# Optimization experiments

Hardware: AMD Instinct MI355X
Metric: run time of the kernel (lower is better)

Reference implementation:

```python
import jax, jax.numpy as jnp
import numpy as np

N = 8192
PERCEPTION = 0.2
SEP_DIST = 0.02
ACC_SCALE = 1.0
ACC_MAX = 1.0
EPS = 1e-08


def setup_inputs() -> dict:
    key = jax.random.key(0)
    k1, k2, k3 = jax.random.split(key, 3)
    position = jax.random.uniform(k1, (N, 2), dtype=jnp.float32)  # boids live in [0,1]^2 torus
    velocity = jax.random.normal(k2, (N, 2), dtype=jnp.float32) * 0.05
    noise = jax.random.uniform(k3, (N, 2), dtype=jnp.float32, minval=-1.0, maxval=1.0)
    return {
        "position": position,
        "velocity": velocity,
        "noise": noise,
        "separation_weight": jnp.float32(4.5),
        "alignment_weight": jnp.float32(0.65),
        "cohesion_weight": jnp.float32(0.75),
        "noise_scale": jnp.float32(0.05),
    }


def _normalize(v):
    # per-row normalize, matching module's _normalize
    norm = jnp.maximum(jnp.linalg.norm(v, axis=-1, keepdims=True), EPS)
    return v / norm


def reference(position, velocity, noise, separation_weight, alignment_weight, cohesion_weight, noise_scale):
    # Toroidal vector from boid i to boid j: diff[i, j, :]  (shape [N, N, 2])
    diff = position[None, :, :] - position[:, None, :]
    diff = jnp.where(diff > 0.5, diff - 1.0, diff)
    diff = jnp.where(diff < -0.5, diff + 1.0, diff)
    dist2 = jnp.sum(diff * diff, axis=-1)  # [N, N]

    not_self = ~jnp.eye(N, dtype=bool)

    # Separation: sum of -toroidal_vector over too-close neighbors, normalized
    sep_mask = not_self & (dist2 <= SEP_DIST ** 2)
    steer_sep = -jnp.sum(jnp.where(sep_mask[..., None], diff, 0.0), axis=1)
    steer_sep = _normalize(steer_sep)

    # Perception mask shared by alignment and cohesion
    perc_mask = not_self & (dist2 <= PERCEPTION ** 2)
    cnt = jnp.sum(perc_mask, axis=1, dtype=position.dtype)[:, None]  # [N, 1]

    # Alignment: mean neighbor velocity minus own velocity, normalized
    vel_avg = jnp.einsum("ij,jd->id", perc_mask.astype(position.dtype), velocity) / cnt
    steer_align = _normalize(vel_avg - velocity)

    # Cohesion: mean toroidal vector to neighbors, normalized
    pos_avg = jnp.sum(jnp.where(perc_mask[..., None], diff, 0.0), axis=1) / cnt
    steer_coh = _normalize(pos_avg)

    acc = (separation_weight * steer_sep
           + alignment_weight * steer_align
           + cohesion_weight * steer_coh)
    acc = acc * ACC_SCALE
    acc = acc + noise_scale * noise

    # clip by norm per boid
    norm = jnp.linalg.norm(acc, axis=-1, keepdims=True)
    acc = jnp.where(norm > ACC_MAX, acc * ACC_MAX / jnp.maximum(norm, EPS), acc)
    return acc
```

## Files before the change

### kernel.cpp

```cpp
#include <hip/hip_runtime.h>
#include <math.h>

#define N_BOIDS 8192
typedef float f32x2 __attribute__((ext_vector_type(2)));
typedef float f32x4 __attribute__((ext_vector_type(4)));

constexpr int   BLOCK           = 256;
constexpr int   WAVES_PER_BLOCK = BLOCK / 64;
constexpr int   I_PER_WAVE      = 2;
constexpr int   I_PER_BLOCK     = WAVES_PER_BLOCK * I_PER_WAVE;
constexpr int   TILE            = 2048;
constexpr int   NTILES          = N_BOIDS / TILE;
constexpr float SEP_R2  = 4.0000000000000008e-04f;
constexpr float PERC_R2 = 4.0000000000000001e-02f;
constexpr float EPSF    = 1e-08f;

__device__ __forceinline__ void finalize_boid(
    int i, const f32x2* __restrict__ vel, const f32x2* __restrict__ noise,
    float ws, float wa, float wc, float wn,
    float sx, float sy, float vx, float vy, float cx, float cy, float cntall,
    float* __restrict__ out)
{
    const float cnt = cntall - 1.0f;

    float ns  = fmaxf(sqrtf(sx * sx + sy * sy), EPSF);
    float ssx = sx / ns, ssy = sy / ns;

    const f32x2 vi = vel[i];
    float vax = (vx - vi.x) / cnt - vi.x;
    float vay = (vy - vi.y) / cnt - vi.y;
    float na  = fmaxf(sqrtf(vax * vax + vay * vay), EPSF);
    float sax = vax / na, say = vay / na;

    float pax = cx / cnt, pay = cy / cnt;
    float nc  = fmaxf(sqrtf(pax * pax + pay * pay), EPSF);
    float scx = pax / nc, scy = pay / nc;

    float ax = ws * ssx + wa * sax + wc * scx;
    float ay = ws * ssy + wa * say + wc * scy;
    const f32x2 nz = noise[i];
    ax += wn * nz.x;
    ay += wn * nz.y;

    const float nn = sqrtf(ax * ax + ay * ay);
    if (nn > 1.0f) {
        const float s = 1.0f / fmaxf(nn, EPSF);
        ax *= s;
        ay *= s;
    }
    out[2 * i]     = ax;
    out[2 * i + 1] = ay;
}

__global__ __launch_bounds__(BLOCK, 4) void boids_kernel(
    const f32x2* __restrict__ pos,
    const f32x2* __restrict__ vel,
    const f32x2* __restrict__ noise,
    const float* __restrict__ w_sep,
    const float* __restrict__ w_ali,
    const float* __restrict__ w_coh,
    const float* __restrict__ w_noise,
    float* __restrict__ out)
{
    __shared__ f32x4 tile[TILE];

    const int tid  = threadIdx.x;
    const int lane = tid & 63;
    const int wid  = tid >> 6;
    const int i0   = (blockIdx.x * WAVES_PER_BLOCK + wid) * I_PER_WAVE;

    const f32x2 P0 = pos[i0];
    const f32x2 P1 = pos[i0 + 1];
    const float vperc = PERC_R2;
    const float vsep  = SEP_R2;

    float n0 = 0.f, s0x = 0.f, s0y = 0.f, v0x = 0.f, v0y = 0.f, c0x = 0.f, c0y = 0.f;
    float n1 = 0.f, s1x = 0.f, s1y = 0.f, v1x = 0.f, v1y = 0.f, c1x = 0.f, c1y = 0.f;

    for (int t = 0; t < NTILES; ++t) {
        const f32x4* gp = reinterpret_cast<const f32x4*>(pos) + t * (TILE / 2);
        const f32x4* gv = reinterpret_cast<const f32x4*>(vel) + t * (TILE / 2);
#pragma unroll
        for (int c = 0; c < TILE / 2 / BLOCK; ++c) {
            const int idx  = tid + c * BLOCK;
            const f32x4 pp = gp[idx];
            const f32x4 vv = gv[idx];
            f32x4 t0; t0.x = pp.x; t0.y = pp.y; t0.z = vv.x; t0.w = vv.y;
            f32x4 t1; t1.x = pp.z; t1.y = pp.w; t1.z = vv.z; t1.w = vv.w;
            tile[2 * idx]     = t0;
            tile[2 * idx + 1] = t1;
        }
        __syncthreads();

#pragma unroll 8
        for (int k = 0; k < TILE / 64; ++k) {
            const f32x4 q = tile[lane + k * 64];
            float dx, dy, ta, tb, m;
            asm(
                "v_sub_f32   %[dx], %[qx], %[p0x]\n\t"
                "v_sub_f32   %[dy], %[qy], %[p0y]\n\t"
                "v_rndne_f32 %[ta], %[dx]\n\t"
                "v_rndne_f32 %[tb], %[dy]\n\t"
                "v_sub_f32   %[dx], %[dx], %[ta]\n\t"
                "v_sub_f32   %[dy], %[dy], %[tb]\n\t"
                "v_mul_f32   %[ta], %[dx], %[dx]\n\t"
                "v_mul_f32   %[tb], %[dy], %[dy]\n\t"
                "v_add_f32   %[ta], %[ta], %[tb]\n\t"
                "v_cmp_ge_f32 vcc, %[vperc], %[ta]\n\t"
                "v_cndmask_b32 %[m], 0, 1.0, vcc\n\t"
                "v_add_f32   %[n0], %[n0], %[m]\n\t"
                "v_fmac_f32  %[v0x], %[m], %[qz]\n\t"
                "v_fmac_f32  %[v0y], %[m], %[qw]\n\t"
                "v_fmac_f32  %[c0x], %[m], %[dx]\n\t"
                "v_fmac_f32  %[c0y], %[m], %[dy]\n\t"
                "v_cmp_ge_f32 vcc, %[vsep], %[ta]\n\t"
                "v_cndmask_b32 %[m], 0, 1.0, vcc\n\t"
                "v_fma_f32   %[s0x], -%[m], %[dx], %[s0x]\n\t"
                "v_fma_f32   %[s0y], -%[m], %[dy], %[s0y]\n\t"
                "v_sub_f32   %[dx], %[qx], %[p1x]\n\t"
                "v_sub_f32   %[dy], %[qy], %[p1y]\n\t"
                "v_rndne_f32 %[ta], %[dx]\n\t"
                "v_rndne_f32 %[tb], %[dy]\n\t"
                "v_sub_f32   %[dx], %[dx], %[ta]\n\t"
                "v_sub_f32   %[dy], %[dy], %[tb]\n\t"
                "v_mul_f32   %[ta], %[dx], %[dx]\n\t"
                "v_mul_f32   %[tb], %[dy], %[dy]\n\t"
                "v_add_f32   %[ta], %[ta], %[tb]\n\t"
                "v_cmp_ge_f32 vcc, %[vperc], %[ta]\n\t"
                "v_cndmask_b32 %[m], 0, 1.0, vcc\n\t"
                "v_add_f32   %[n1], %[n1], %[m]\n\t"
                "v_fmac_f32  %[v1x], %[m], %[qz]\n\t"
                "v_fmac_f32  %[v1y], %[m], %[qw]\n\t"
                "v_fmac_f32  %[c1x], %[m], %[dx]\n\t"
                "v_fmac_f32  %[c1y], %[m], %[dy]\n\t"
                "v_cmp_ge_f32 vcc, %[vsep], %[ta]\n\t"
                "v_cndmask_b32 %[m], 0, 1.0, vcc\n\t"
                "v_fma_f32   %[s1x], -%[m], %[dx], %[s1x]\n\t"
                "v_fma_f32   %[s1y], -%[m], %[dy], %[s1y]\n\t"
                : [dx] "=&v"(dx), [dy] "=&v"(dy), [ta] "=&v"(ta),
                  [tb] "=&v"(tb), [m] "=&v"(m),
                  [n0] "+v"(n0), [s0x] "+v"(s0x), [s0y] "+v"(s0y),
                  [v0x] "+v"(v0x), [v0y] "+v"(v0y), [c0x] "+v"(c0x), [c0y] "+v"(c0y),
                  [n1] "+v"(n1), [s1x] "+v"(s1x), [s1y] "+v"(s1y),
                  [v1x] "+v"(v1x), [v1y] "+v"(v1y), [c1x] "+v"(c1x), [c1y] "+v"(c1y)
                : [qx] "v"(q.x), [qy] "v"(q.y), [qz] "v"(q.z), [qw] "v"(q.w),
                  [p0x] "v"(P0.x), [p0y] "v"(P0.y),
                  [p1x] "v"(P1.x), [p1y] "v"(P1.y),
                  [vperc] "v"(vperc), [vsep] "v"(vsep)
                : "vcc");
        }
        __syncthreads();
    }

#pragma unroll
    for (int mlev = 1; mlev < 64; mlev <<= 1) {
        n0  += __shfl_xor(n0,  mlev);
        s0x += __shfl_xor(s0x, mlev);  s0y += __shfl_xor(s0y, mlev);
        v0x += __shfl_xor(v0x, mlev);  v0y += __shfl_xor(v0y, mlev);
        c0x += __shfl_xor(c0x, mlev);  c0y += __shfl_xor(c0y, mlev);
        n1  += __shfl_xor(n1,  mlev);
        s1x += __shfl_xor(s1x, mlev);  s1y += __shfl_xor(s1y, mlev);
        v1x += __shfl_xor(v1x, mlev);  v1y += __shfl_xor(v1y, mlev);
        c1x += __shfl_xor(c1x, mlev);  c1y += __shfl_xor(c1y, mlev);
    }

    float sx = s0x, sy = s0y, vx = v0x, vy = v0y, cx = c0x, cy = c0y, cc = n0;
    if (lane == 1) {
        sx = s1x; sy = s1y; vx = v1x; vy = v1y; cx = c1x; cy = c1y; cc = n1;
    }
    if (lane < I_PER_WAVE) {
        const float ws = w_sep[0], wa = w_ali[0], wc = w_coh[0], wn = w_noise[0];
        finalize_boid(i0 + lane, vel, noise, ws, wa, wc, wn,
                      sx, sy, vx, vy, cx, cy, cc, out);
    }
}

extern "C" void kernel_launch(void* const* d_in, const int* in_sizes, int n_in,
                              void* d_out, int out_size, void* d_ws, size_t ws_size,
                              hipStream_t stream) {
    const f32x2* pos     = (const f32x2*)d_in[0];
    const f32x2* vel     = (const f32x2*)d_in[1];
    const f32x2* noise   = (const f32x2*)d_in[2];
    const float* w_sep   = (const float*)d_in[3];
    const float* w_ali   = (const float*)d_in[4];
    const float* w_coh   = (const float*)d_in[5];
    const float* w_noise = (const float*)d_in[6];
    float* out = (float*)d_out;

    const int grid = N_BOIDS / I_PER_BLOCK;
    boids_kernel<<<grid, BLOCK, 0, stream>>>(pos, vel, noise, w_sep, w_ali,
                                             w_coh, w_noise, out);
}
```

Before: 34.26 us.

## Split neighbor loop across wave pairs and branch-skip sparse separation updates

```diff
diff --git a/kernel.cpp b/kernel.cpp
--- a/kernel.cpp
+++ b/kernel.cpp
@@ -5,12 +5,14 @@
 typedef float f32x2 __attribute__((ext_vector_type(2)));
 typedef float f32x4 __attribute__((ext_vector_type(4)));
 
-constexpr int   BLOCK           = 256;
-constexpr int   WAVES_PER_BLOCK = BLOCK / 64;
-constexpr int   I_PER_WAVE      = 2;
-constexpr int   I_PER_BLOCK     = WAVES_PER_BLOCK * I_PER_WAVE;
-constexpr int   TILE            = 2048;
-constexpr int   NTILES          = N_BOIDS / TILE;
+constexpr int   BLOCK       = 1024;
+constexpr int   JSPLIT      = 2;
+constexpr int   GROUPS      = (BLOCK / 64) / JSPLIT;
+constexpr int   I_PER_GROUP = 2;
+constexpr int   I_PER_BLOCK = GROUPS * I_PER_GROUP;
+constexpr int   TILE        = 4096;
+constexpr int   NTILES      = N_BOIDS / TILE;
+constexpr int   K_PER_WAVE  = TILE / 64 / JSPLIT;
 constexpr float SEP_R2  = 4.0000000000000008e-04f;
 constexpr float PERC_R2 = 4.0000000000000001e-02f;
 constexpr float EPSF    = 1e-08f;
@@ -52,7 +54,7 @@
     out[2 * i + 1] = ay;
 }
 
-__global__ __launch_bounds__(BLOCK, 4) void boids_kernel(
+__global__ __launch_bounds__(BLOCK, 8) void boids_kernel(
     const f32x2* __restrict__ pos,
     const f32x2* __restrict__ vel,
     const f32x2* __restrict__ noise,
@@ -63,19 +65,22 @@
     float* __restrict__ out)
 {
     __shared__ f32x4 tile[TILE];
+    __shared__ float comb[GROUPS][16];
 
     const int tid  = threadIdx.x;
     const int lane = tid & 63;
     const int wid  = tid >> 6;
-    const int i0   = (blockIdx.x * WAVES_PER_BLOCK + wid) * I_PER_WAVE;
+    const int g    = wid >> 1;
+    const int h    = wid & 1;
+    const int i0   = blockIdx.x * I_PER_BLOCK + g * I_PER_GROUP;
 
     const f32x2 P0 = pos[i0];
     const f32x2 P1 = pos[i0 + 1];
     const float vperc = PERC_R2;
     const float vsep  = SEP_R2;
 
-    float n0 = 0.f, s0x = 0.f, s0y = 0.f, v0x = 0.f, v0y = 0.f, c0x = 0.f, c0y = 0.f;
-    float n1 = 0.f, s1x = 0.f, s1y = 0.f, v1x = 0.f, v1y = 0.f, c1x = 0.f, c1y = 0.f;
+    float n0  = 0.f, s0x = 0.f, s0y = 0.f, v0x = 0.f, v0y = 0.f, c0x = 0.f, c0y = 0.f;
+    float n1  = 0.f, s1x = 0.f, s1y = 0.f, v1x = 0.f, v1y = 0.f, c1x = 0.f, c1y = 0.f;
 
     for (int t = 0; t < NTILES; ++t) {
         const f32x4* gp = reinterpret_cast<const f32x4*>(pos) + t * (TILE / 2);
@@ -92,62 +97,71 @@
         }
         __syncthreads();
 
+        const int kbase = h * K_PER_WAVE;
 #pragma unroll 8
-        for (int k = 0; k < TILE / 64; ++k) {
-            const f32x4 q = tile[lane + k * 64];
-            float dx, dy, ta, tb, m;
+        for (int k = 0; k < K_PER_WAVE; ++k) {
+            const f32x4 q = tile[lane + (kbase + k) * 64];
+            float dx0, dy0, dx1, dy1, ta, tb, tc, m;
+            unsigned long long ka, kb, kc;
             asm(
-                "v_sub_f32   %[dx], %[qx], %[p0x]\n\t"
-                "v_sub_f32   %[dy], %[qy], %[p0y]\n\t"
-                "v_rndne_f32 %[ta], %[dx]\n\t"
-                "v_rndne_f32 %[tb], %[dy]\n\t"
-                "v_sub_f32   %[dx], %[dx], %[ta]\n\t"
-                "v_sub_f32   %[dy], %[dy], %[tb]\n\t"
-                "v_mul_f32   %[ta], %[dx], %[dx]\n\t"
-                "v_mul_f32   %[tb], %[dy], %[dy]\n\t"
+                "v_sub_f32   %[dx0], %[qx], %[p0x]\n\t"
+                "v_sub_f32   %[dy0], %[qy], %[p0y]\n\t"
+                "v_sub_f32   %[dx1], %[qx], %[p1x]\n\t"
+                "v_sub_f32   %[dy1], %[qy], %[p1y]\n\t"
+                "v_rndne_f32 %[ta], %[dx0]\n\t"
+                "v_rndne_f32 %[tb], %[dy0]\n\t"
+                "v_sub_f32   %[dx0], %[dx0], %[ta]\n\t"
+                "v_sub_f32   %[dy0], %[dy0], %[tb]\n\t"
+                "v_rndne_f32 %[ta], %[dx1]\n\t"
+                "v_rndne_f32 %[tb], %[dy1]\n\t"
+                "v_sub_f32   %[dx1], %[dx1], %[ta]\n\t"
+                "v_sub_f32   %[dy1], %[dy1], %[tb]\n\t"
+                "v_mul_f32   %[ta], %[dx0], %[dx0]\n\t"
+                "v_mul_f32   %[tb], %[dy0], %[dy0]\n\t"
                 "v_add_f32   %[ta], %[ta], %[tb]\n\t"
+                "v_mul_f32   %[tb], %[dx1], %[dx1]\n\t"
+                "v_mul_f32   %[tc], %[dy1], %[dy1]\n\t"
+                "v_add_f32   %[tb], %[tb], %[tc]\n\t"
                 "v_cmp_ge_f32 vcc, %[vperc], %[ta]\n\t"
                 "v_cndmask_b32 %[m], 0, 1.0, vcc\n\t"
                 "v_add_f32   %[n0], %[n0], %[m]\n\t"
                 "v_fmac_f32  %[v0x], %[m], %[qz]\n\t"
                 "v_fmac_f32  %[v0y], %[m], %[qw]\n\t"
-                "v_fmac_f32  %[c0x], %[m], %[dx]\n\t"
-                "v_fmac_f32  %[c0y], %[m], %[dy]\n\t"
-                "v_cmp_ge_f32 vcc, %[vsep], %[ta]\n\t"
-                "v_cndmask_b32 %[m], 0, 1.0, vcc\n\t"
-                "v_fma_f32   %[s0x], -%[m], %[dx], %[s0x]\n\t"
-                "v_fma_f32   %[s0y], -%[m], %[dy], %[s0y]\n\t"
-                "v_sub_f32   %[dx], %[qx], %[p1x]\n\t"
-                "v_sub_f32   %[dy], %[qy], %[p1y]\n\t"
-                "v_rndne_f32 %[ta], %[dx]\n\t"
-                "v_rndne_f32 %[tb], %[dy]\n\t"
-                "v_sub_f32   %[dx], %[dx], %[ta]\n\t"
-                "v_sub_f32   %[dy], %[dy], %[tb]\n\t"
-                "v_mul_f32   %[ta], %[dx], %[dx]\n\t"
-                "v_mul_f32   %[tb], %[dy], %[dy]\n\t"
-                "v_add_f32   %[ta], %[ta], %[tb]\n\t"
-                "v_cmp_ge_f32 vcc, %[vperc], %[ta]\n\t"
+                "v_fmac_f32  %[c0x], %[m], %[dx0]\n\t"
+                "v_fmac_f32  %[c0y], %[m], %[dy0]\n\t"
+                "v_cmp_ge_f32 vcc, %[vperc], %[tb]\n\t"
                 "v_cndmask_b32 %[m], 0, 1.0, vcc\n\t"
                 "v_add_f32   %[n1], %[n1], %[m]\n\t"
                 "v_fmac_f32  %[v1x], %[m], %[qz]\n\t"
                 "v_fmac_f32  %[v1y], %[m], %[qw]\n\t"
-                "v_fmac_f32  %[c1x], %[m], %[dx]\n\t"
-                "v_fmac_f32  %[c1y], %[m], %[dy]\n\t"
-                "v_cmp_ge_f32 vcc, %[vsep], %[ta]\n\t"
-                "v_cndmask_b32 %[m], 0, 1.0, vcc\n\t"
-                "v_fma_f32   %[s1x], -%[m], %[dx], %[s1x]\n\t"
-                "v_fma_f32   %[s1y], -%[m], %[dy], %[s1y]\n\t"
-                : [dx] "=&v"(dx), [dy] "=&v"(dy), [ta] "=&v"(ta),
-                  [tb] "=&v"(tb), [m] "=&v"(m),
+                "v_fmac_f32  %[c1x], %[m], %[dx1]\n\t"
+                "v_fmac_f32  %[c1y], %[m], %[dy1]\n\t"
+                "v_cmp_ge_f32 %[ka], %[vsep], %[ta]\n\t"
+                "v_cmp_ge_f32 %[kb], %[vsep], %[tb]\n\t"
+                "s_or_b64    %[kc], %[ka], %[kb]\n\t"
+                "s_cbranch_scc0 Lsep%=\n\t"
+                "v_cndmask_b32 %[m], 0, 1.0, %[ka]\n\t"
+                "v_fma_f32   %[s0x], -%[m], %[dx0], %[s0x]\n\t"
+                "v_fma_f32   %[s0y], -%[m], %[dy0], %[s0y]\n\t"
+                "v_cndmask_b32 %[m], 0, 1.0, %[kb]\n\t"
+                "v_fma_f32   %[s1x], -%[m], %[dx1], %[s1x]\n\t"
+                "v_fma_f32   %[s1y], -%[m], %[dy1], %[s1y]\n\t"
+                "Lsep%=:"
+                : [dx0] "=&v"(dx0), [dy0] "=&v"(dy0),
+                  [dx1] "=&v"(dx1), [dy1] "=&v"(dy1),
+                  [ta] "=&v"(ta), [tb] "=&v"(tb), [tc] "=&v"(tc), [m] "=&v"(m),
+                  [ka] "=&s"(ka), [kb] "=&s"(kb), [kc] "=&s"(kc),
                   [n0] "+v"(n0), [s0x] "+v"(s0x), [s0y] "+v"(s0y),
-                  [v0x] "+v"(v0x), [v0y] "+v"(v0y), [c0x] "+v"(c0x), [c0y] "+v"(c0y),
+                  [v0x] "+v"(v0x), [v0y] "+v"(v0y),
+                  [c0x] "+v"(c0x), [c0y] "+v"(c0y),
                   [n1] "+v"(n1), [s1x] "+v"(s1x), [s1y] "+v"(s1y),
-                  [v1x] "+v"(v1x), [v1y] "+v"(v1y), [c1x] "+v"(c1x), [c1y] "+v"(c1y)
+                  [v1x] "+v"(v1x), [v1y] "+v"(v1y),
+                  [c1x] "+v"(c1x), [c1y] "+v"(c1y)
                 : [qx] "v"(q.x), [qy] "v"(q.y), [qz] "v"(q.z), [qw] "v"(q.w),
                   [p0x] "v"(P0.x), [p0y] "v"(P0.y),
                   [p1x] "v"(P1.x), [p1y] "v"(P1.y),
                   [vperc] "v"(vperc), [vsep] "v"(vsep)
-                : "vcc");
+                : "vcc", "scc");
         }
         __syncthreads();
     }
@@ -164,11 +178,26 @@
         c1x += __shfl_xor(c1x, mlev);  c1y += __shfl_xor(c1y, mlev);
     }
 
-    float sx = s0x, sy = s0y, vx = v0x, vy = v0y, cx = c0x, cy = c0y, cc = n0;
-    if (lane == 1) {
-        sx = s1x; sy = s1y; vx = v1x; vy = v1y; cx = c1x; cy = c1y; cc = n1;
-    }
-    if (lane < I_PER_WAVE) {
+    if (h == 1 && lane == 0) {
+        comb[g][0]  = s0x; comb[g][1]  = s0y;
+        comb[g][2]  = v0x; comb[g][3]  = v0y;
+        comb[g][4]  = c0x; comb[g][5]  = c0y;
+        comb[g][6]  = n0;
+        comb[g][7]  = s1x; comb[g][8]  = s1y;
+        comb[g][9]  = v1x; comb[g][10] = v1y;
+        comb[g][11] = c1x; comb[g][12] = c1y;
+        comb[g][13] = n1;
+    }
+    __syncthreads();
+
+    if (h == 0 && lane < I_PER_GROUP) {
+        float sx = s0x, sy = s0y, vx = v0x, vy = v0y, cx = c0x, cy = c0y, cc = n0;
+        if (lane == 1) {
+            sx = s1x; sy = s1y; vx = v1x; vy = v1y; cx = c1x; cy = c1y; cc = n1;
+        }
+        const float* cb = &comb[g][lane * 7];
+        sx += cb[0]; sy += cb[1]; vx += cb[2]; vy += cb[3];
+        cx += cb[4]; cy += cb[5]; cc += cb[6];
         const float ws = w_sep[0], wa = w_ali[0], wc = w_coh[0], wn = w_noise[0];
         finalize_boid(i0 + lane, vel, noise, ws, wa, wc, wn,
                       sx, sy, vx, vy, cx, cy, cc, out);
```

Measured after the change: 35.47 us. 1.04x slower.
